# Kernel tuning notes

Hardware: AMD Instinct MI355X
Metric: run time of the kernel (lower is better)

The kernel has to match this reference:

```python
import jax, jax.numpy as jnp
import numpy as np
import math

N, E, D, H = 50000, 1600000, 128, 8
DH = D // H  # per-head dim
EPS = 1e-5   # batchnorm eps


def _attn(q_in, k_in, v_in, Wq, Wk, Wv, src, dst):
    # GAT-style edge attention: score = exp(clip(<K[src],Q[dst]>/sqrt(DH), -5, 5))
    Q = (q_in @ Wq.T).reshape(-1, H, DH)
    K = (k_in @ Wk.T).reshape(-1, H, DH)
    V = (v_in @ Wv.T).reshape(-1, H, DH)
    score = jnp.exp(jnp.clip((K[src] * Q[dst]).sum(-1) / math.sqrt(DH), -5.0, 5.0))  # [E,H]
    wV = jax.ops.segment_sum(V[src] * score[:, :, None], dst, num_segments=N)  # [N,H,DH]
    z = jax.ops.segment_sum(score, dst, num_segments=N)                         # [N,H]
    return (wV / z[:, :, None]).reshape(-1, D)


def _bn(x, gamma, beta):
    # BatchNorm1d in training mode: biased batch stats over nodes
    m = x.mean(0)
    v = x.var(0)
    return (x - m) / jnp.sqrt(v + EPS) * gamma + beta


def setup_inputs() -> dict:
    key = jax.random.key(0)
    ks = iter(jax.random.split(key, 48))

    def w(shape, scale=None):
        s = scale if scale is not None else 1.0 / math.sqrt(shape[-1])
        return jax.random.normal(next(ks), shape, jnp.float32) * s

    inp = dict(
        h=w((N, D), 1.0),
        sv=w((N, D), 1.0),
        src=jax.random.randint(next(ks), (E,), 0, N, jnp.int32),
        dst=jax.random.randint(next(ks), (E,), 0, N, jnp.int32),
    )
    for nm in ["Wq_sv", "Wk_sv", "Wv_sv", "Wq_cv", "Wk_cv", "Wv_cv",
               "Wq_sh", "Wk_sh", "Wv_sh"]:
        inp[nm] = w((D, D))
    inp.update(
        Wo=w((D, 2 * D)), bo=jnp.zeros((D,), jnp.float32),
        Wo_h=w((D, 2 * D)), bo_h=jnp.zeros((D,), jnp.float32),
        W1=w((2 * D, D)), b1=jnp.zeros((2 * D,), jnp.float32),
        W2=w((D, 2 * D)), b2=jnp.zeros((D,), jnp.float32),
        W1h=w((2 * D, D)), b1h=jnp.zeros((2 * D,), jnp.float32),
        W2h=w((D, 2 * D)), b2h=jnp.zeros((D,), jnp.float32),
        Wg1=w((D, D)), bg1=jnp.zeros((D,), jnp.float32),
        Wg2=w((D, D)), bg2=jnp.zeros((D,), jnp.float32),
        gbn1=jnp.ones((D,), jnp.float32), bbn1=jnp.zeros((D,), jnp.float32),
        gbn2=jnp.ones((D,), jnp.float32), bbn2=jnp.zeros((D,), jnp.float32),
        gbn1h=jnp.ones((D,), jnp.float32), bbn1h=jnp.zeros((D,), jnp.float32),
        gbn2h=jnp.ones((D,), jnp.float32), bbn2h=jnp.zeros((D,), jnp.float32),
    )
    return inp


def reference(h, sv, src, dst,
              Wq_sv, Wk_sv, Wv_sv, Wq_cv, Wk_cv, Wv_cv, Wq_sh, Wk_sh, Wv_sh,
              Wo, bo, Wo_h, bo_h,
              W1, b1, W2, b2, W1h, b1h, W2h, b2h,
              Wg1, bg1, Wg2, bg2,
              gbn1, bbn1, gbn2, bbn2, gbn1h, bbn1h, gbn2h, bbn2h):
    h_in1, sv_in1 = h, sv
    # --- h branch ---
    a_self = _attn(h, h, h, Wq_sv, Wk_sv, Wv_sv, src, dst)
    a_cross = _attn(h, sv, sv, Wq_cv, Wk_cv, Wv_cv, src, dst)
    hO = jnp.concatenate([a_self, a_cross], -1) @ Wo.T + bo
    h1 = _bn(h_in1 + hO, gbn1, bbn1)
    ffn = jax.nn.relu(h1 @ W1.T + b1) @ W2.T + b2
    h_out = _bn(h1 + ffn, gbn2, bbn2)
    # --- state-vector branch ---
    a_self_h = _attn(sv, sv, sv, Wq_sh, Wk_sh, Wv_sh, src, dst)
    # faithful to source: cross_attention_v weights reused here
    a_cross_h = _attn(sv, h_in1, h_in1, Wq_cv, Wk_cv, Wv_cv, src, dst)
    svO = jnp.concatenate([a_self_h, a_cross_h], -1) @ Wo_h.T + bo_h
    g1 = jax.nn.sigmoid(h_in1 @ Wg1.T + bg1)
    sv1 = _bn((1.0 - g1) * sv_in1 + g1 * svO, gbn1h, bbn1h)
    ffn_h = jax.nn.relu(sv1 @ W1h.T + b1h) @ W2h.T + b2h
    g2 = jax.nn.sigmoid(h_in1 @ Wg2.T + bg2)
    sv_out = _bn((1.0 - g2) * sv1 + g2 * ffn_h, gbn2h, bbn2h)
    return (h_out, sv_out)
```

## Files before the change

### kernel.cpp

```cpp
#include <hip/hip_runtime.h>

typedef _Float16 f16x8 __attribute__((ext_vector_type(8)));
typedef _Float16 f16x2 __attribute__((ext_vector_type(2)));
typedef __fp16 fp16x2_raw __attribute__((ext_vector_type(2)));
typedef float f32x4 __attribute__((ext_vector_type(4)));
typedef float f32x2 __attribute__((ext_vector_type(2)));
typedef unsigned int uint32;
typedef unsigned short ushort16;
typedef unsigned char uchar;

#define EPS_BN 1e-5f

__device__ __forceinline__ uint32 pk16(float a, float b){
  fp16x2_raw h = __builtin_amdgcn_cvt_pkrtz(a, b);
  return *(uint32*)&h;
}
__device__ __forceinline__ uchar f2fp8(float f){
  uint32 p = __builtin_amdgcn_cvt_pk_fp8_f32(f, f, 0, false);
  return (uchar)(p & 0xff);
}
__device__ __forceinline__ f32x2 fp8pair_lo(uint32 w){
  return __builtin_amdgcn_cvt_pk_f32_fp8(w, false);
}
__device__ __forceinline__ f32x2 fp8pair_hi(uint32 w){
  return __builtin_amdgcn_cvt_pk_f32_fp8(w, true);
}

struct WEnt { const float* s; const float* s2; ushort16* d; int KD, MD, nfrag; };
struct WConv { WEnt e[16]; };

__global__ __launch_bounds__(256) void prep_k(WConv wc,
    const float* __restrict__ a, const float* __restrict__ b,
    ushort16* __restrict__ da, ushort16* __restrict__ db, int n,
    const int* __restrict__ dst, int* __restrict__ bcnt, int E, int shift){
  int y = blockIdx.y;
  if (y < 2){
    const float* s = y ? b : a;
    ushort16* d = y ? db : da;
    int i = (blockIdx.x * 256 + threadIdx.x) * 4;
    if (i >= n) return;
    float4 v = *(const float4*)(s + i);
    uint2 p;
    p.x = pk16(v.x, v.y);
    p.y = pk16(v.z, v.w);
    *(uint2*)(d + i) = p;
  } else if (y == 2){
    __shared__ int lh[128];
    if (blockIdx.x >= 512) return;
    int tid = threadIdx.x;
    if (tid < 128) lh[tid] = 0;
    __syncthreads();
    int stride = 512 * 256;
    for (int i = blockIdx.x * 256 + tid; i < E; i += stride)
      atomicAdd(&lh[dst[i] >> shift], 1);
    __syncthreads();
    if (tid < 128 && lh[tid]) atomicAdd(&bcnt[tid], lh[tid]);
  } else {
    if (blockIdx.x >= 256) return;
    WEnt t = wc.e[blockIdx.x >> 4];
    int fid = (blockIdx.x & 15) * 256 + threadIdx.x;
    if (fid >= t.nfrag) return;
    int lane = fid & 63, sm = fid >> 6;
    int MT = t.MD >> 4;
    int s = sm / MT, m = sm - s * MT;
    int row = m * 16 + (lane & 15);
    int col = s * 32 + (lane >> 4) * 8;
    const float* sp = t.s;
    if (t.s2 && row >= 128){ sp = t.s2; row -= 128; }
    const float* p = sp + (size_t)row * t.KD + col;
    uint4 o;
    o.x = pk16(p[0], p[1]); o.y = pk16(p[2], p[3]);
    o.z = pk16(p[4], p[5]); o.w = pk16(p[6], p[7]);
    *(uint4*)(t.d + (size_t)fid * 8) = o;
  }
}

__global__ __launch_bounds__(64) void bscan_k(const int* __restrict__ bcnt,
    int* __restrict__ bstart, int* __restrict__ bcur, int B){
  if (threadIdx.x == 0){
    int run = 0;
    for (int b = 0; b < B; b++){ bstart[b] = run; bcur[b] = run; run += bcnt[b]; }
    bstart[B] = run;
  }
}

#define BIN_TB 512
#define BIN_TILE 4096
__global__ __launch_bounds__(512) void bin_k(const int* __restrict__ src, const int* __restrict__ dst,
                                             int* __restrict__ bcur, uint2* __restrict__ ebuf,
                                             int E, int shift, int B){
  __shared__ int lhist[128];
  __shared__ int lstart[128];
  __shared__ int gbase[128];
  __shared__ uint2 lpair[BIN_TILE];
  int tid = threadIdx.x;
  int base = blockIdx.x * BIN_TILE;
  int cnt = E - base; if (cnt > BIN_TILE) cnt = BIN_TILE;
  if (tid < 128) lhist[tid] = 0;
  __syncthreads();
  int myb[8], myrank[8];
  uint2 myp[8];
  int nmine = 0;
  #pragma unroll
  for (int j = 0; j < 8; j++){
    int i = tid + j * BIN_TB;
    if (i < cnt){
      int s = src[base + i], d = dst[base + i];
      int b = d >> shift;
      myp[nmine] = make_uint2((uint32)s, (uint32)d);
      myb[nmine] = b;
      myrank[nmine] = atomicAdd(&lhist[b], 1);
      nmine++;
    }
  }
  __syncthreads();
  if (tid == 0){
    int run = 0;
    for (int b = 0; b < B; b++){ lstart[b] = run; run += lhist[b]; }
  }
  __syncthreads();
  if (tid < B) gbase[tid] = atomicAdd(&bcur[tid], lhist[tid]);
  for (int j = 0; j < nmine; j++){
    lpair[lstart[myb[j]] + myrank[j]] = myp[j];
  }
  __syncthreads();
  for (int i = tid; i < cnt; i += BIN_TB){
    uint2 p = lpair[i];
    int b = (int)(p.y >> shift);
    ebuf[gbase[b] + (i - lstart[b])] = p;
  }
}

#define CSR_TB 1024
__global__ __launch_bounds__(1024) void csr_k(const uint2* __restrict__ ebuf,
    const int* __restrict__ bstart, int* __restrict__ row_off, int* __restrict__ esrc,
    int shift, int N, int E, int B){
  __shared__ int lc[4096];
  __shared__ int lcur[4096];
  __shared__ int wsum[16];
  int b = blockIdx.x;
  int d0 = b << shift;
  int nd = 1 << shift; if (d0 + nd > N) nd = N - d0;
  if (nd <= 0) return;
  int e0 = bstart[b], e1 = bstart[b + 1];
  int tid = threadIdx.x, lane = tid & 63, wv = tid >> 6;
  for (int j = tid; j < nd; j += CSR_TB){ lc[j] = 0; lcur[j] = 0; }
  __syncthreads();
  for (int i = e0 + tid; i < e1; i += CSR_TB){
    atomicAdd(&lc[(int)ebuf[i].y - d0], 1);
  }
  __syncthreads();
  int base4 = tid * 4;
  int v0 = (base4 + 0 < nd) ? lc[base4 + 0] : 0;
  int v1 = (base4 + 1 < nd) ? lc[base4 + 1] : 0;
  int v2 = (base4 + 2 < nd) ? lc[base4 + 2] : 0;
  int v3 = (base4 + 3 < nd) ? lc[base4 + 3] : 0;
  int ts = v0 + v1 + v2 + v3;
  int inc = ts;
  #pragma unroll
  for (int d = 1; d < 64; d <<= 1){
    int t = __shfl_up(inc, d);
    if (lane >= d) inc += t;
  }
  if (lane == 63) wsum[wv] = inc;
  __syncthreads();
  int woff = 0;
  for (int w = 0; w < 16; w++) if (w < wv) woff += wsum[w];
  int excl = woff + (inc - ts);
  int o0 = excl, o1 = o0 + v0, o2 = o1 + v1, o3 = o2 + v2;
  __syncthreads();
  if (base4 + 0 < nd){ lc[base4 + 0] = o0; row_off[d0 + base4 + 0] = e0 + o0; }
  if (base4 + 1 < nd){ lc[base4 + 1] = o1; row_off[d0 + base4 + 1] = e0 + o1; }
  if (base4 + 2 < nd){ lc[base4 + 2] = o2; row_off[d0 + base4 + 2] = e0 + o2; }
  if (base4 + 3 < nd){ lc[base4 + 3] = o3; row_off[d0 + base4 + 3] = e0 + o3; }
  __syncthreads();
  for (int i = e0 + tid; i < e1; i += CSR_TB){
    uint2 p = ebuf[i];
    int d = (int)p.y - d0;
    int r = atomicAdd(&lcur[d], 1);
    esrc[e0 + lc[d] + r] = (int)p.x;
  }
  if (b == B - 1 && tid == 0) row_off[N] = E;
}

template<int KD, int MD, int EPI, int ABN, int ST, int GS>
__device__ __forceinline__ void gemm_body(
    const ushort16* __restrict__ X, const ushort16* __restrict__ W,
    const float* __restrict__ bias, const float* __restrict__ bias2,
    const ushort16* __restrict__ resb, const ushort16* __restrict__ gatep,
    const float* __restrict__ rstats, const float* __restrict__ rg, const float* __restrict__ rb,
    const float* __restrict__ astats, const float* __restrict__ ag, const float* __restrict__ ab,
    ushort16* __restrict__ outb, float* __restrict__ stats_out, int N, float invN,
    _Float16* OsBase, float* sstB, float* sst2B)
{
  constexpr int KS = KD / 32;
  constexpr int MT = MD / 16;
  constexpr int LSTR = MD + 8;
  int lane = threadIdx.x & 63, wv = threadIdx.x >> 6;
  _Float16* OsW = OsBase + wv * 16 * LSTR;
  int l15 = lane & 15, kq = lane >> 4;
  int rowbase = (blockIdx.x * 4 + wv) * 16;
  int row = rowbase + l15;
  int rc = row < N ? row : N - 1;
  const f16x8* ap = (const f16x8*)(X + (size_t)rc * KD + kq * 8);
  f16x8 a[KS];
  #pragma unroll
  for (int s = 0; s < KS; s++) a[s] = ap[s * 4];
  if constexpr (ABN){
    #pragma unroll
    for (int s = 0; s < KS; s++){
      #pragma unroll
      for (int j = 0; j < 8; j++){
        int c = s * 32 + kq * 8 + j;
        float mm = astats[c] * invN;
        float var = astats[128 + c] * invN - mm * mm;
        float rs = rsqrtf(var + EPS_BN);
        float scc = rs * ag[c];
        float shh = ab[c] - mm * scc;
        a[s][j] = (_Float16)((float)a[s][j] * scc + shh);
      }
    }
  }
  const f16x8* Wf = (const f16x8*)W;
  f32x4 acc[MT];
  #pragma unroll
  for (int m = 0; m < MT; m++) acc[m] = (f32x4)(0.f);
  #pragma unroll
  for (int s = 0; s < KS; s++){
    #pragma unroll
    for (int m = 0; m < MT; m++){
      acc[m] = __builtin_amdgcn_mfma_f32_16x16x32_f16(a[s], Wf[(s * MT + m) * 64 + lane], acc[m], 0, 0, 0);
    }
  }
  float ps[MT], ps2[MT];
  if constexpr (ST){
    #pragma unroll
    for (int m = 0; m < MT; m++){ ps[m] = 0.f; ps2[m] = 0.f; }
  }
  int r0 = rowbase + kq * 4;
  #pragma unroll
  for (int m = 0; m < MT; m++){
    int col = m * 16 + l15;
    float bv;
    if (bias2 && col >= 128) bv = bias2[col - 128];
    else bv = bias[col];
    float sc = 0.f, sh = 0.f;
    if constexpr (EPI == 5 || EPI == 6){
      float mm = rstats[col] * invN;
      float var = rstats[128 + col] * invN - mm * mm;
      float rs = rsqrtf(var + EPS_BN);
      sc = rs * rg[col]; sh = rb[col] - mm * sc;
    }
    #pragma unroll
    for (int r = 0; r < 4; r++){
      int rr = r0 + r;
      float v;
      {
        int rrc = rr < N ? rr : N - 1;
        v = acc[m][r] + bv;
        if constexpr (EPI == 1) v = fmaxf(v, 0.f);
        if constexpr (EPI == 2) v = 1.f / (1.f + __expf(-v));
        if constexpr (EPI == 3){
          union { ushort16 u; _Float16 h; } cv; cv.u = resb[(size_t)rrc * 128 + col];
          v += (float)cv.h;
        }
        if constexpr (EPI == 5){
          union { ushort16 u; _Float16 h; } cv; cv.u = resb[(size_t)rrc * 128 + col];
          v += (float)cv.h * sc + sh;
        }
        if constexpr (EPI == 4 || EPI == 6){
          union { ushort16 u; _Float16 h; } gv; gv.u = gatep[(size_t)rrc * GS + col];
          union { ushort16 u; _Float16 h; } cv; cv.u = resb[(size_t)rrc * 128 + col];
          float g = (float)gv.h;
          float rv = (float)cv.h;
          if constexpr (EPI == 6) rv = rv * sc + sh;
          v = (1.f - g) * rv + g * v;
        }
      }
      OsW[(kq * 4 + r) * LSTR + col] = (_Float16)v;
      if constexpr (ST){
        if (rr < N){ ps[m] += v; ps2[m] += v * v; }
      }
    }
  }
  if constexpr (MD == 128){
    #pragma unroll
    for (int p = 0; p < 4; p++){
      int lrow = p * 4 + (lane >> 4);
      int rr = rowbase + lrow;
      int col8 = l15 * 8;
      if (rr < N){
        uint4 ov = *(uint4*)&OsW[lrow * LSTR + col8];
        *(uint4*)(outb + (size_t)rr * MD + col8) = ov;
      }
    }
  } else {
    #pragma unroll
    for (int p = 0; p < 8; p++){
      int lrow = p * 2 + (lane >> 5);
      int rr = rowbase + lrow;
      int col8 = (lane & 31) * 8;
      if (rr < N){
        uint4 ov = *(uint4*)&OsW[lrow * LSTR + col8];
        *(uint4*)(outb + (size_t)rr * MD + col8) = ov;
      }
    }
  }
  if constexpr (ST){
    #pragma unroll
    for (int m = 0; m < MT; m++){
      float s = ps[m], s2 = ps2[m];
      s  += __shfl_xor(s, 16);  s  += __shfl_xor(s, 32);
      s2 += __shfl_xor(s2, 16); s2 += __shfl_xor(s2, 32);
      if (lane < 16){ sstB[wv * 128 + m * 16 + l15] = s; sst2B[wv * 128 + m * 16 + l15] = s2; }
    }
    __syncthreads();
    int tid = threadIdx.x;
    if (tid < 128){
      atomicAdd(&stats_out[tid], sstB[tid] + sstB[128 + tid] + sstB[256 + tid] + sstB[384 + tid]);
    } else {
      int c = tid - 128;
      atomicAdd(&stats_out[tid], sst2B[c] + sst2B[128 + c] + sst2B[256 + c] + sst2B[384 + c]);
    }
  }
}

template<int KD, int MD, int EPI, int ABN, int ST, int GS>
__global__ __launch_bounds__(256) void gemm_k(
    const ushort16* __restrict__ X, const ushort16* __restrict__ W,
    const float* __restrict__ bias, const float* __restrict__ bias2,
    const ushort16* __restrict__ resb, const ushort16* __restrict__ gatep,
    const float* __restrict__ rstats, const float* __restrict__ rg, const float* __restrict__ rb,
    const float* __restrict__ astats, const float* __restrict__ ag, const float* __restrict__ ab,
    ushort16* __restrict__ outb, float* __restrict__ stats_out, int N, float invN)
{
  __shared__ _Float16 Os[4 * 16 * (MD + 8)];
  __shared__ float sst[512];
  __shared__ float sst2[512];
  gemm_body<KD, MD, EPI, ABN, ST, GS>(X, W, bias, bias2, resb, gatep, rstats, rg, rb,
                                      astats, ag, ab, outb, stats_out, N, invN, Os, sst, sst2);
}

struct QkvArgs {
  const ushort16* Xq[4];
  const ushort16* Xkv[4];
  const ushort16* Wq[4];
  const ushort16* Wk[4];
  const ushort16* Wv[4];
  ushort16* Qo[4];
};
__global__ __launch_bounds__(256) void qkv_k(QkvArgs A, uchar* __restrict__ KV8, int N)
{
  __shared__ _Float16 S[4][16 * 136];
  int slot = blockIdx.y;
  int toff = slot << 8;
  const ushort16* Xq = A.Xq[slot];
  const ushort16* Xkv = A.Xkv[slot];
  ushort16* Qo = A.Qo[slot];
  int lane = threadIdx.x & 63, wv = threadIdx.x >> 6;
  _Float16* SW = S[wv];
  uchar* SB = (uchar*)SW;
  int l15 = lane & 15, kq = lane >> 4;
  int rowbase = (blockIdx.x * 4 + wv) * 16;
  int row = rowbase + l15;
  int rc = row < N ? row : N - 1;
  const f16x8* aq = (const f16x8*)(Xq + (size_t)rc * 128 + kq * 8);
  const f16x8* ak = (const f16x8*)(Xkv + (size_t)rc * 128 + kq * 8);
  f16x8 Aq[4], Ak[4];
  #pragma unroll
  for (int s = 0; s < 4; s++){ Aq[s] = aq[s * 4]; Ak[s] = ak[s * 4]; }
  const f16x8* Wqf = (const f16x8*)A.Wq[slot];
  const f16x8* Wkf = (const f16x8*)A.Wk[slot];
  const f16x8* Wvf = (const f16x8*)A.Wv[slot];
  f32x4 acc[8];

  #pragma unroll
  for (int m = 0; m < 8; m++) acc[m] = (f32x4)(0.f);
  #pragma unroll
  for (int s = 0; s < 4; s++){
    #pragma unroll
    for (int m = 0; m < 8; m++){
      acc[m] = __builtin_amdgcn_mfma_f32_16x16x32_f16(Aq[s], Wqf[(s * 8 + m) * 64 + lane], acc[m], 0, 0, 0);
    }
  }
  #pragma unroll
  for (int m = 0; m < 8; m++){
    int col = m * 16 + l15;
    #pragma unroll
    for (int r = 0; r < 4; r++)
      SW[(kq * 4 + r) * 136 + col] = (_Float16)acc[m][r];
  }
  #pragma unroll
  for (int p = 0; p < 4; p++){
    int lrow = p * 4 + kq;
    int rr = rowbase + lrow;
    int col8 = l15 * 8;
    if (rr < N){
      uint4 qv = *(uint4*)&SW[lrow * 136 + col8];
      *(uint4*)(Qo + (size_t)rr * 128 + col8) = qv;
    }
  }

  #pragma unroll
  for (int m = 0; m < 8; m++) acc[m] = (f32x4)(0.f);
  #pragma unroll
  for (int s = 0; s < 4; s++){
    #pragma unroll
    for (int m = 0; m < 8; m++){
      acc[m] = __builtin_amdgcn_mfma_f32_16x16x32_f16(Ak[s], Wkf[(s * 8 + m) * 64 + lane], acc[m], 0, 0, 0);
    }
  }
  #pragma unroll
  for (int m = 0; m < 8; m++){
    int col = m * 16 + l15;
    #pragma unroll
    for (int r = 0; r < 4; r++)
      SB[(kq * 4 + r) * 136 + col] = f2fp8(acc[m][r]);
  }
  #pragma unroll
  for (int p = 0; p < 4; p++){
    int lrow = p * 4 + kq;
    int rr = rowbase + lrow;
    int col8 = l15 * 8;
    if (rr < N){
      uint2 kv = *(uint2*)&SB[lrow * 136 + col8];
      *(uint2*)(KV8 + (size_t)rr * 1024 + toff + col8) = kv;
    }
  }

  #pragma unroll
  for (int m = 0; m < 8; m++) acc[m] = (f32x4)(0.f);
  #pragma unroll
  for (int s = 0; s < 4; s++){
    #pragma unroll
    for (int m = 0; m < 8; m++){
      acc[m] = __builtin_amdgcn_mfma_f32_16x16x32_f16(Ak[s], Wvf[(s * 8 + m) * 64 + lane], acc[m], 0, 0, 0);
    }
  }
  #pragma unroll
  for (int m = 0; m < 8; m++){
    int col = m * 16 + l15;
    #pragma unroll
    for (int r = 0; r < 4; r++)
      SB[(kq * 4 + r) * 136 + col] = f2fp8(acc[m][r]);
  }
  #pragma unroll
  for (int p = 0; p < 4; p++){
    int lrow = p * 4 + kq;
    int rr = rowbase + lrow;
    int col8 = l15 * 8;
    if (rr < N){
      uint2 vv = *(uint2*)&SB[lrow * 136 + col8];
      *(uint2*)(KV8 + (size_t)rr * 1024 + toff + 128 + col8) = vv;
    }
  }
}

struct GPairArgs {
  const ushort16* X[2]; const ushort16* W[2];
  const float* bias[2];
  const ushort16* resb[2]; const ushort16* gatep[2];
  const float* rstats[2]; const float* rg[2]; const float* rb[2];
  const float* astats[2]; const float* ag[2]; const float* ab[2];
  ushort16* outb[2]; float* stats_out[2];
};
template<int KD, int MD, int EPI0, int EPI1, int ABN, int ST, int GS>
__global__ __launch_bounds__(256) void gemm_pair_k(GPairArgs A, int N, float invN)
{
  __shared__ _Float16 Os[4 * 16 * (MD + 8)];
  __shared__ float sst[512];
  __shared__ float sst2[512];
  int y = blockIdx.y;
  if (y == 0){
    gemm_body<KD, MD, EPI0, ABN, ST, GS>(A.X[0], A.W[0], A.bias[0], nullptr, A.resb[0], A.gatep[0],
        A.rstats[0], A.rg[0], A.rb[0], A.astats[0], A.ag[0], A.ab[0],
        A.outb[0], A.stats_out[0], N, invN, Os, sst, sst2);
  } else {
    gemm_body<KD, MD, EPI1, ABN, ST, GS>(A.X[1], A.W[1], A.bias[1], nullptr, A.resb[1], A.gatep[1],
        A.rstats[1], A.rg[1], A.rb[1], A.astats[1], A.ag[1], A.ab[1],
        A.outb[1], A.stats_out[1], N, invN, Os, sst, sst2);
  }
}

__global__ __launch_bounds__(256) void attn4_k(
    const ushort16* __restrict__ Qa, const ushort16* __restrict__ Qb,
    const ushort16* __restrict__ Qc, const ushort16* __restrict__ Qd,
    const uchar* __restrict__ KV,
    const int* __restrict__ row_off, const int* __restrict__ esrc,
    ushort16* __restrict__ cat_h, ushort16* __restrict__ cat_sv, int n0, int n1)
{
  int wv = threadIdx.x >> 6, lane = threadIdx.x & 63;
  int n = n0 + blockIdx.x * 4 + wv;
  if (n >= n1) return;
  int g = lane >> 4, j = lane & 15;
  uint32 j8 = (uint32)j * 8u;
  const float QS = 0.25f * 1.44269504088896f;
  const float CL = 7.21347520444482f;
  const ushort16* Qp[4] = {Qa, Qb, Qc, Qd};
  f32x2 q[4][4];
  #pragma unroll
  for (int t = 0; t < 4; t++){
    uint4 u = *(const uint4*)(Qp[t] + (size_t)n * 128 + j8);
    f16x2 h0 = *(f16x2*)&u.x, h1 = *(f16x2*)&u.y;
    f16x2 h2 = *(f16x2*)&u.z, h3 = *(f16x2*)&u.w;
    q[t][0].x = (float)h0.x * QS; q[t][0].y = (float)h0.y * QS;
    q[t][1].x = (float)h1.x * QS; q[t][1].y = (float)h1.y * QS;
    q[t][2].x = (float)h2.x * QS; q[t][2].y = (float)h2.y * QS;
    q[t][3].x = (float)h3.x * QS; q[t][3].y = (float)h3.y * QS;
  }
  int e0 = row_off[n], e1 = row_off[n + 1];
  int itmax = (e1 - e0 + 3) >> 2;
  f32x2 ac[4][4];
  #pragma unroll
  for (int t = 0; t < 4; t++){
    #pragma unroll
    for (int r = 0; r < 4; r++) ac[t][r] = (f32x2)(0.f);
  }
  float z[4] = {0.f, 0.f, 0.f, 0.f};
  int e = e0 + g;
  int s = (e < e1) ? esrc[e] : -1;
  uint32 off = ((uint32)(s < 0 ? 0 : s) << 10) + j8;
  uint2 kc[4], vc[4];
  #pragma unroll
  for (int t = 0; t < 4; t++){
    kc[t] = *(const uint2*)(KV + off + t * 256);
    vc[t] = *(const uint2*)(KV + off + t * 256 + 128);
  }
  for (int it = 0; it < itmax; ++it){
    int e2 = e + 4;
    int s2 = (e2 < e1) ? esrc[e2] : -1;
    uint32 off2 = ((uint32)(s2 < 0 ? 0 : s2) << 10) + j8;
    uint2 kn[4], vn[4];
    #pragma unroll
    for (int t = 0; t < 4; t++){
      kn[t] = *(const uint2*)(KV + off2 + t * 256);
      vn[t] = *(const uint2*)(KV + off2 + t * 256 + 128);
    }
    if (s >= 0){
      #pragma unroll
      for (int t = 0; t < 4; t++){
        f32x2 k0 = fp8pair_lo(kc[t].x), k1 = fp8pair_hi(kc[t].x);
        f32x2 k2 = fp8pair_lo(kc[t].y), k3 = fp8pair_hi(kc[t].y);
        f32x2 dd = k0 * q[t][0] + k1 * q[t][1] + k2 * q[t][2] + k3 * q[t][3];
        float d = dd.x + dd.y;
        d += __shfl_xor(d, 1);
        float sc = __builtin_amdgcn_exp2f(__builtin_amdgcn_fmed3f(d, -CL, CL));
        f32x2 v0 = fp8pair_lo(vc[t].x), v1 = fp8pair_hi(vc[t].x);
        f32x2 v2 = fp8pair_lo(vc[t].y), v3 = fp8pair_hi(vc[t].y);
        f32x2 sv; sv.x = sc; sv.y = sc;
        ac[t][0] += sv * v0; ac[t][1] += sv * v1;
        ac[t][2] += sv * v2; ac[t][3] += sv * v3;
        z[t] += sc;
      }
    }
    e = e2; s = s2; off = off2;
    #pragma unroll
    for (int t = 0; t < 4; t++){ kc[t] = kn[t]; vc[t] = vn[t]; }
  }
  #pragma unroll
  for (int t = 0; t < 4; t++){
    #pragma unroll
    for (int r = 0; r < 4; r++){
      ac[t][r].x += __shfl_xor(ac[t][r].x, 16);
      ac[t][r].y += __shfl_xor(ac[t][r].y, 16);
      ac[t][r].x += __shfl_xor(ac[t][r].x, 32);
      ac[t][r].y += __shfl_xor(ac[t][r].y, 32);
    }
    z[t] += __shfl_xor(z[t], 16);
    z[t] += __shfl_xor(z[t], 32);
  }
  if (g == 0){
    size_t base = (size_t)n * 256 + j8;
    #pragma unroll
    for (int t = 0; t < 4; t++){
      float rz = __builtin_amdgcn_rcpf(z[t]);
      uint4 o;
      o.x = pk16(ac[t][0].x * rz, ac[t][0].y * rz);
      o.y = pk16(ac[t][1].x * rz, ac[t][1].y * rz);
      o.z = pk16(ac[t][2].x * rz, ac[t][2].y * rz);
      o.w = pk16(ac[t][3].x * rz, ac[t][3].y * rz);
      ushort16* dp = (t < 2) ? cat_h : cat_sv;
      *(uint4*)(dp + base + (t & 1) * 128) = o;
    }
  }
}

struct Bn2Args {
  const ushort16* x[2]; const float* stats[2];
  const float* g[2]; const float* b[2]; float* out[2];
};
__global__ __launch_bounds__(256) void bn2_k(Bn2Args A, int total4, float invN)
{
  int y = blockIdx.y;
  int i = blockIdx.x * 256 + threadIdx.x;
  if (i >= total4) return;
  const ushort16* x = A.x[y];
  const float* stats = A.stats[y];
  const float* gamma = A.g[y];
  const float* beta = A.b[y];
  float* outf = A.out[y];
  uint2 xp = *(const uint2*)(x + (size_t)i * 4);
  f16x2 x01 = *(f16x2*)&xp.x, x23 = *(f16x2*)&xp.y;
  float xv[4] = {(float)x01.x, (float)x01.y, (float)x23.x, (float)x23.y};
  int c0 = (i * 4) & 127;
  float o[4];
  #pragma unroll
  for (int j = 0; j < 4; j++){
    int c = c0 + j;
    float m = stats[c] * invN;
    float var = stats[128 + c] * invN - m * m;
    float rstd = rsqrtf(var + EPS_BN);
    o[j] = (xv[j] - m) * rstd * gamma[c] + beta[c];
  }
  *(float4*)(outf + (size_t)i * 4) = make_float4(o[0], o[1], o[2], o[3]);
}

extern "C" void kernel_launch(void* const* d_in, const int* in_sizes, int n_in,
                              void* d_out, int out_size, void* d_ws, size_t ws_size,
                              hipStream_t stream) {
  const float* h   = (const float*)d_in[0];
  const float* sv  = (const float*)d_in[1];
  const int* src   = (const int*)d_in[2];
  const int* dst   = (const int*)d_in[3];
  const int N = in_sizes[0] / 128;
  const int E = in_sizes[2];

  char* wsb = (char*)d_ws;
  size_t o = 0;
  auto take = [&](size_t bytes)->size_t{
    size_t r = o;
    o = (o + bytes + 255) & ~(size_t)255;
    return r;
  };
  size_t big = (size_t)E * 8;
  if (big < (size_t)N * 1024) big = (size_t)N * 1024;
  size_t bcnt_off   = take(128 * 4);
  size_t stats_off  = take(4 * 256 * 4);
  size_t bstart_off = take(132 * 4);
  size_t bcur_off   = take(128 * 4);
  size_t rowoff_off = take((size_t)(N + 1) * 4);
  size_t esrc_off   = take((size_t)E * 4);
  size_t big_off    = take(big);
  size_t wpool_off  = take((size_t)376832 * 2);
  size_t hf_off     = take((size_t)N * 128 * 2);
  size_t svf_off    = take((size_t)N * 128 * 2);
  size_t cath_off   = take((size_t)N * 256 * 2);
  size_t catsv_off  = take((size_t)N * 256 * 2);
  size_t Q1_off     = take((size_t)N * 128 * 2);
  size_t Q2_off     = take((size_t)N * 128 * 2);
  size_t X1_off     = take((size_t)N * 128 * 2);
  size_t X2_off     = take((size_t)N * 128 * 2);
  size_t G_off      = take((size_t)N * 256 * 2);

  int*    bcnt    = (int*)(wsb + bcnt_off);
  float*  stats   = (float*)(wsb + stats_off);
  int*    bstart  = (int*)(wsb + bstart_off);
  int*    bcur    = (int*)(wsb + bcur_off);
  int*    row_off = (int*)(wsb + rowoff_off);
  int*    esrc    = (int*)(wsb + esrc_off);
  uint2*  ebuf    = (uint2*)(wsb + big_off);
  uchar*  KVall   = (uchar*)(wsb + big_off);
  ushort16* wpool = (ushort16*)(wsb + wpool_off);
  ushort16* h_f   = (ushort16*)(wsb + hf_off);
  ushort16* sv_f  = (ushort16*)(wsb + svf_off);
  ushort16* cat_h = (ushort16*)(wsb + cath_off);
  ushort16* cat_sv= (ushort16*)(wsb + catsv_off);
  ushort16* Q1    = (ushort16*)(wsb + Q1_off);
  ushort16* Q2    = (ushort16*)(wsb + Q2_off);
  ushort16* Xb1   = (ushort16*)(wsb + X1_off);
  ushort16* Xb2   = (ushort16*)(wsb + X2_off);
  ushort16* Gbuf  = (ushort16*)(wsb + G_off);
  ushort16* Q3 = Xb1;
  ushort16* Q4 = Xb2;

  ushort16* Wq_sv = wpool + 0 * 16384;
  ushort16* Wk_sv = wpool + 1 * 16384;
  ushort16* Wv_sv = wpool + 2 * 16384;
  ushort16* Wq_cv = wpool + 3 * 16384;
  ushort16* Wk_cv = wpool + 4 * 16384;
  ushort16* Wv_cv = wpool + 5 * 16384;
  ushort16* Wq_sh = wpool + 6 * 16384;
  ushort16* Wk_sh = wpool + 7 * 16384;
  ushort16* Wv_sh = wpool + 8 * 16384;
  ushort16* Wgb   = wpool + 147456;
  ushort16* Wob   = wpool + 180224;
  ushort16* Wohb  = wpool + 212992;
  ushort16* W1b   = wpool + 245760;
  ushort16* W2b   = wpool + 278528;
  ushort16* W1hb  = wpool + 311296;
  ushort16* W2hb  = wpool + 344064;

  const float* bo   = (const float*)d_in[14];
  const float* bo_h = (const float*)d_in[16];
  const float* b1   = (const float*)d_in[18];
  const float* b2   = (const float*)d_in[20];
  const float* b1h  = (const float*)d_in[22];
  const float* b2h  = (const float*)d_in[24];
  const float* bg1  = (const float*)d_in[26];
  const float* bg2  = (const float*)d_in[28];
  const float* gbn1  = (const float*)d_in[29];
  const float* bbn1  = (const float*)d_in[30];
  const float* gbn2  = (const float*)d_in[31];
  const float* bbn2  = (const float*)d_in[32];
  const float* gbn1h = (const float*)d_in[33];
  const float* bbn1h = (const float*)d_in[34];
  const float* gbn2h = (const float*)d_in[35];
  const float* bbn2h = (const float*)d_in[36];

  float* out_h  = (float*)d_out;
  float* out_sv = out_h + (size_t)N * 128;

  (void)hipMemsetAsync(wsb, 0, stats_off + 4 * 256 * 4, stream);

  WConv wc;
  {
    auto set = [&](int i, int din, int din2, size_t dstoff, int KD, int MD){
      wc.e[i].s  = (const float*)d_in[din];
      wc.e[i].s2 = (din2 >= 0) ? (const float*)d_in[din2] : nullptr;
      wc.e[i].d  = wpool + dstoff;
      wc.e[i].KD = KD; wc.e[i].MD = MD;
      wc.e[i].nfrag = KD * MD / 8;
    };
    for (int i = 0; i < 9; i++) set(i, 4 + i, -1, (size_t)i * 16384, 128, 128);
    set(9,  25, 27, 147456, 128, 256);
    set(10, 13, -1, 180224, 256, 128);
    set(11, 15, -1, 212992, 256, 128);
    set(12, 17, -1, 245760, 128, 256);
    set(13, 19, -1, 278528, 256, 128);
    set(14, 21, -1, 311296, 128, 256);
    set(15, 23, -1, 344064, 256, 128);
  }

  int shift = 9;
  while ((((N - 1) >> shift) + 1) > 128) shift++;
  const int B = ((N - 1) >> shift) + 1;

  int nelem = N * 128;
  int CVB = (nelem / 4 + 255) / 256;
  int PXB = CVB > 512 ? CVB : 512;
  prep_k<<<dim3(PXB, 4), 256, 0, stream>>>(wc, h, sv, h_f, sv_f, nelem, dst, bcnt, E, shift);

  bscan_k<<<1, 64, 0, stream>>>(bcnt, bstart, bcur, B);
  bin_k<<<(E + BIN_TILE - 1) / BIN_TILE, BIN_TB, 0, stream>>>(src, dst, bcur, ebuf, E, shift, B);
  csr_k<<<B, CSR_TB, 0, stream>>>(ebuf, bstart, row_off, esrc, shift, N, E, B);

  const int GB = (N + 63) / 64;
  const int AB = (N + 3) / 4;
  const int T4 = nelem / 4;
  const int APB = (T4 + 255) / 256;
  const float invN = 1.f / (float)N;

  gemm_k<128,256,2,0,0,256><<<GB, 256, 0, stream>>>(h_f, Wgb, bg1, bg2, nullptr, nullptr,
      nullptr, nullptr, nullptr, nullptr, nullptr, nullptr, Gbuf, nullptr, N, invN);

  QkvArgs qa;
  qa.Xq[0] = h_f;  qa.Xkv[0] = h_f;  qa.Wq[0] = Wq_sv; qa.Wk[0] = Wk_sv; qa.Wv[0] = Wv_sv; qa.Qo[0] = Q1;
  qa.Xq[1] = h_f;  qa.Xkv[1] = sv_f; qa.Wq[1] = Wq_cv; qa.Wk[1] = Wk_cv; qa.Wv[1] = Wv_cv; qa.Qo[1] = Q2;
  qa.Xq[2] = sv_f; qa.Xkv[2] = sv_f; qa.Wq[2] = Wq_sh; qa.Wk[2] = Wk_sh; qa.Wv[2] = Wv_sh; qa.Qo[2] = Q3;
  qa.Xq[3] = sv_f; qa.Xkv[3] = h_f;  qa.Wq[3] = Wq_cv; qa.Wk[3] = Wk_cv; qa.Wv[3] = Wv_cv; qa.Qo[3] = Q4;
  qkv_k<<<dim3(GB, 4), 256, 0, stream>>>(qa, KVall, N);
  attn4_k<<<AB, 256, 0, stream>>>(Q1, Q2, Q3, Q4, KVall, row_off, esrc, cat_h, cat_sv, 0, N);

  {
    GPairArgs A = {};
    A.X[0] = cat_h;  A.W[0] = Wob;  A.bias[0] = bo;   A.resb[0] = h_f;  A.gatep[0] = nullptr;
    A.outb[0] = Xb1; A.stats_out[0] = stats;
    A.X[1] = cat_sv; A.W[1] = Wohb; A.bias[1] = bo_h; A.resb[1] = sv_f; A.gatep[1] = Gbuf;
    A.outb[1] = Q1;  A.stats_out[1] = stats + 512;
    gemm_pair_k<256,128,3,4,0,1,256><<<dim3(GB, 2), 256, 0, stream>>>(A, N, invN);
  }
  {
    GPairArgs A = {};
    A.X[0] = Xb1; A.W[0] = W1b;  A.bias[0] = b1;
    A.astats[0] = stats;       A.ag[0] = gbn1;  A.ab[0] = bbn1;  A.outb[0] = cat_h;
    A.X[1] = Q1;  A.W[1] = W1hb; A.bias[1] = b1h;
    A.astats[1] = stats + 512; A.ag[1] = gbn1h; A.ab[1] = bbn1h; A.outb[1] = cat_sv;
    gemm_pair_k<128,256,1,1,1,0,256><<<dim3(GB, 2), 256, 0, stream>>>(A, N, invN);
  }
  {
    GPairArgs A = {};
    A.X[0] = cat_h;  A.W[0] = W2b;  A.bias[0] = b2;  A.resb[0] = Xb1;
    A.rstats[0] = stats;       A.rg[0] = gbn1;  A.rb[0] = bbn1;
    A.outb[0] = Xb2; A.stats_out[0] = stats + 256;
    A.X[1] = cat_sv; A.W[1] = W2hb; A.bias[1] = b2h; A.resb[1] = Q1;  A.gatep[1] = Gbuf + 128;
    A.rstats[1] = stats + 512; A.rg[1] = gbn1h; A.rb[1] = bbn1h;
    A.outb[1] = Q2;  A.stats_out[1] = stats + 768;
    gemm_pair_k<256,128,5,6,0,1,256><<<dim3(GB, 2), 256, 0, stream>>>(A, N, invN);
  }
  {
    Bn2Args A;
    A.x[0] = Xb2; A.stats[0] = stats + 256; A.g[0] = gbn2;  A.b[0] = bbn2;  A.out[0] = out_h;
    A.x[1] = Q2;  A.stats[1] = stats + 768; A.g[1] = gbn2h; A.b[1] = bbn2h; A.out[1] = out_sv;
    bn2_k<<<dim3(APB, 2), 256, 0, stream>>>(A, T4, invN);
  }
}
```

Before: 722.9 us.

## Split prep kernel, stage QKV weights in LDS, chunk attention launch

Splits the combined prep kernel into a separate fp32-to-fp16 conversion kernel and an auxiliary histogram/weight-fragment kernel, so no blocks are launched only to exit early. The QKV projection kernel now copies each 128x128 fp16 weight matrix into shared memory once per block and reads MFMA fragments from LDS instead of global memory. This costs extra barriers and 32KB of LDS, which may lower occupancy. The attention kernel is launched as three node-range chunks instead of one grid, possibly to improve cache locality or scheduling, at the price of extra launch overhead.

```diff
diff --git a/kernel.cpp b/kernel.cpp
--- a/kernel.cpp
+++ b/kernel.cpp
@@ -29,36 +29,36 @@
 struct WEnt { const float* s; const float* s2; ushort16* d; int KD, MD, nfrag; };
 struct WConv { WEnt e[16]; };
 
-__global__ __launch_bounds__(256) void prep_k(WConv wc,
-    const float* __restrict__ a, const float* __restrict__ b,
-    ushort16* __restrict__ da, ushort16* __restrict__ db, int n,
+__global__ __launch_bounds__(256) void conv2_k(const float* __restrict__ a, const float* __restrict__ b,
+                                               ushort16* __restrict__ da, ushort16* __restrict__ db, int n){
+  const float* s = blockIdx.y ? b : a;
+  ushort16* d = blockIdx.y ? db : da;
+  int i = (blockIdx.x * 256 + threadIdx.x) * 4;
+  if (i >= n) return;
+  float4 v = *(const float4*)(s + i);
+  uint2 p;
+  p.x = pk16(v.x, v.y);
+  p.y = pk16(v.z, v.w);
+  *(uint2*)(d + i) = p;
+}
+
+__global__ __launch_bounds__(256) void aux_k(WConv wc,
     const int* __restrict__ dst, int* __restrict__ bcnt, int E, int shift){
-  int y = blockIdx.y;
-  if (y < 2){
-    const float* s = y ? b : a;
-    ushort16* d = y ? db : da;
-    int i = (blockIdx.x * 256 + threadIdx.x) * 4;
-    if (i >= n) return;
-    float4 v = *(const float4*)(s + i);
-    uint2 p;
-    p.x = pk16(v.x, v.y);
-    p.y = pk16(v.z, v.w);
-    *(uint2*)(d + i) = p;
-  } else if (y == 2){
+  int bx = blockIdx.x;
+  if (bx < 512){
     __shared__ int lh[128];
-    if (blockIdx.x >= 512) return;
     int tid = threadIdx.x;
     if (tid < 128) lh[tid] = 0;
     __syncthreads();
     int stride = 512 * 256;
-    for (int i = blockIdx.x * 256 + tid; i < E; i += stride)
+    for (int i = bx * 256 + tid; i < E; i += stride)
       atomicAdd(&lh[dst[i] >> shift], 1);
     __syncthreads();
     if (tid < 128 && lh[tid]) atomicAdd(&bcnt[tid], lh[tid]);
   } else {
-    if (blockIdx.x >= 256) return;
-    WEnt t = wc.e[blockIdx.x >> 4];
-    int fid = (blockIdx.x & 15) * 256 + threadIdx.x;
+    int b = bx - 512;
+    WEnt t = wc.e[b >> 4];
+    int fid = (b & 15) * 256 + threadIdx.x;
     if (fid >= t.nfrag) return;
     int lane = fid & 63, sm = fid >> 6;
     int MT = t.MD >> 4;
@@ -351,13 +351,15 @@
 };
 __global__ __launch_bounds__(256) void qkv_k(QkvArgs A, uchar* __restrict__ KV8, int N)
 {
+  __shared__ _Float16 Wl[16384];
   __shared__ _Float16 S[4][16 * 136];
   int slot = blockIdx.y;
   int toff = slot << 8;
   const ushort16* Xq = A.Xq[slot];
   const ushort16* Xkv = A.Xkv[slot];
   ushort16* Qo = A.Qo[slot];
-  int lane = threadIdx.x & 63, wv = threadIdx.x >> 6;
+  int tid = threadIdx.x;
+  int lane = tid & 63, wv = tid >> 6;
   _Float16* SW = S[wv];
   uchar* SB = (uchar*)SW;
   int l15 = lane & 15, kq = lane >> 4;
@@ -369,18 +371,28 @@
   f16x8 Aq[4], Ak[4];
   #pragma unroll
   for (int s = 0; s < 4; s++){ Aq[s] = aq[s * 4]; Ak[s] = ak[s * 4]; }
-  const f16x8* Wqf = (const f16x8*)A.Wq[slot];
-  const f16x8* Wkf = (const f16x8*)A.Wk[slot];
-  const f16x8* Wvf = (const f16x8*)A.Wv[slot];
+  const uint4* Wq4 = (const uint4*)A.Wq[slot];
+  const uint4* Wk4 = (const uint4*)A.Wk[slot];
+  const uint4* Wv4 = (const uint4*)A.Wv[slot];
+  uint4* Wl4 = (uint4*)Wl;
+  const f16x8* Wl8 = (const f16x8*)Wl;
   f32x4 acc[8];
 
+  {
+    uint4 wb[8];
+    #pragma unroll
+    for (int r = 0; r < 8; r++) wb[r] = Wq4[tid + r * 256];
+    #pragma unroll
+    for (int r = 0; r < 8; r++) Wl4[tid + r * 256] = wb[r];
+  }
+  __syncthreads();
   #pragma unroll
   for (int m = 0; m < 8; m++) acc[m] = (f32x4)(0.f);
   #pragma unroll
   for (int s = 0; s < 4; s++){
     #pragma unroll
     for (int m = 0; m < 8; m++){
-      acc[m] = __builtin_amdgcn_mfma_f32_16x16x32_f16(Aq[s], Wqf[(s * 8 + m) * 64 + lane], acc[m], 0, 0, 0);
+      acc[m] = __builtin_amdgcn_mfma_f32_16x16x32_f16(Aq[s], Wl8[(s * 8 + m) * 64 + lane], acc[m], 0, 0, 0);
     }
   }
   #pragma unroll
@@ -400,14 +412,23 @@
       *(uint4*)(Qo + (size_t)rr * 128 + col8) = qv;
     }
   }
-
+  __syncthreads();
+
+  {
+    uint4 wb[8];
+    #pragma unroll
+    for (int r = 0; r < 8; r++) wb[r] = Wk4[tid + r * 256];
+    #pragma unroll
+    for (int r = 0; r < 8; r++) Wl4[tid + r * 256] = wb[r];
+  }
+  __syncthreads();
   #pragma unroll
   for (int m = 0; m < 8; m++) acc[m] = (f32x4)(0.f);
   #pragma unroll
   for (int s = 0; s < 4; s++){
     #pragma unroll
     for (int m = 0; m < 8; m++){
-      acc[m] = __builtin_amdgcn_mfma_f32_16x16x32_f16(Ak[s], Wkf[(s * 8 + m) * 64 + lane], acc[m], 0, 0, 0);
+      acc[m] = __builtin_amdgcn_mfma_f32_16x16x32_f16(Ak[s], Wl8[(s * 8 + m) * 64 + lane], acc[m], 0, 0, 0);
     }
   }
   #pragma unroll
@@ -427,14 +448,23 @@
       *(uint2*)(KV8 + (size_t)rr * 1024 + toff + col8) = kv;
     }
   }
-
+  __syncthreads();
+
+  {
+    uint4 wb[8];
+    #pragma unroll
+    for (int r = 0; r < 8; r++) wb[r] = Wv4[tid + r * 256];
+    #pragma unroll
+    for (int r = 0; r < 8; r++) Wl4[tid + r * 256] = wb[r];
+  }
+  __syncthreads();
   #pragma unroll
   for (int m = 0; m < 8; m++) acc[m] = (f32x4)(0.f);
   #pragma unroll
   for (int s = 0; s < 4; s++){
     #pragma unroll
     for (int m = 0; m < 8; m++){
-      acc[m] = __builtin_amdgcn_mfma_f32_16x16x32_f16(Ak[s], Wvf[(s * 8 + m) * 64 + lane], acc[m], 0, 0, 0);
+      acc[m] = __builtin_amdgcn_mfma_f32_16x16x32_f16(Ak[s], Wl8[(s * 8 + m) * 64 + lane], acc[m], 0, 0, 0);
     }
   }
   #pragma unroll
@@ -737,15 +767,14 @@
 
   int nelem = N * 128;
   int CVB = (nelem / 4 + 255) / 256;
-  int PXB = CVB > 512 ? CVB : 512;
-  prep_k<<<dim3(PXB, 4), 256, 0, stream>>>(wc, h, sv, h_f, sv_f, nelem, dst, bcnt, E, shift);
+  conv2_k<<<dim3(CVB, 2), 256, 0, stream>>>(h, sv, h_f, sv_f, nelem);
+  aux_k<<<768, 256, 0, stream>>>(wc, dst, bcnt, E, shift);
 
   bscan_k<<<1, 64, 0, stream>>>(bcnt, bstart, bcur, B);
   bin_k<<<(E + BIN_TILE - 1) / BIN_TILE, BIN_TB, 0, stream>>>(src, dst, bcur, ebuf, E, shift, B);
   csr_k<<<B, CSR_TB, 0, stream>>>(ebuf, bstart, row_off, esrc, shift, N, E, B);
 
   const int GB = (N + 63) / 64;
-  const int AB = (N + 3) / 4;
   const int T4 = nelem / 4;
   const int APB = (T4 + 255) / 256;
   const float invN = 1.f / (float)N;
@@ -759,7 +788,15 @@
   qa.Xq[2] = sv_f; qa.Xkv[2] = sv_f; qa.Wq[2] = Wq_sh; qa.Wk[2] = Wk_sh; qa.Wv[2] = Wv_sh; qa.Qo[2] = Q3;
   qa.Xq[3] = sv_f; qa.Xkv[3] = h_f;  qa.Wq[3] = Wq_cv; qa.Wk[3] = Wk_cv; qa.Wv[3] = Wv_cv; qa.Qo[3] = Q4;
   qkv_k<<<dim3(GB, 4), 256, 0, stream>>>(qa, KVall, N);
-  attn4_k<<<AB, 256, 0, stream>>>(Q1, Q2, Q3, Q4, KVall, row_off, esrc, cat_h, cat_sv, 0, N);
+
+  {
+    int per = ((N + 2) / 3 + 3) & ~3;
+    for (int n0 = 0; n0 < N; n0 += per){
+      int n1 = n0 + per; if (n1 > N) n1 = N;
+      attn4_k<<<(n1 - n0 + 3) / 4, 256, 0, stream>>>(Q1, Q2, Q3, Q4, KVall,
+                                                     row_off, esrc, cat_h, cat_sv, n0, n1);
+    }
+  }
 
   {
     GPairArgs A = {};
```

Measured after the change: 725.8 us. Within noise of the previous version (+0.4%).
